# Performance work log

Measured on AMD Instinct MI355X. Metric: run time of the kernel, lower is better.

The kernel has to match this reference:

```python
import jax, jax.numpy as jnp
import numpy as np

E, C_IN, NUM_CLASSES = 4, 3, 100
HW = 32
C1, C2, GC = 64, 128, 16
FC_IN = C2 * (HW // 4) * (HW // 4)  # 128*8*8 = 8192


def _conv(x, w, b):
    # x: [B,Cin,H,W], w: [Cout,Cin,3,3] -> [B,Cout,H,W] (SAME padding)
    y = jax.lax.conv_general_dilated(x, w, (1, 1), 'SAME',
                                     dimension_numbers=('NCHW', 'OIHW', 'NCHW'))
    return y + b[None, :, None, None]


def _maxpool2(x):
    return jax.lax.reduce_window(x, -jnp.inf, jax.lax.max,
                                 (1, 1, 2, 2), (1, 1, 2, 2), 'VALID')


def setup_inputs() -> dict:
    key = jax.random.key(0)
    ks = jax.random.split(key, 12)
    s = lambda k, shape, fan: (jax.random.normal(k, shape, jnp.float32) / np.sqrt(fan))
    return {
        'x': jax.random.normal(ks[0], (1024, C_IN, HW, HW), jnp.float32),
        # gating network
        'gate_cw': s(ks[1], (GC, C_IN, 3, 3), C_IN * 9),
        'gate_cb': jnp.zeros((GC,), jnp.float32),
        'gate_fw': s(ks[2], (E, GC), GC),
        'gate_fb': jnp.zeros((E,), jnp.float32),
        # stacked expert params [E, ...]
        'e_c1w': s(ks[3], (E, C1, C_IN, 3, 3), C_IN * 9),
        'e_c1b': jnp.zeros((E, C1), jnp.float32),
        'e_c2w': s(ks[4], (E, C2, C1, 3, 3), C1 * 9),
        'e_c2b': jnp.zeros((E, C2), jnp.float32),
        'e_fw': s(ks[5], (E, NUM_CLASSES, FC_IN), FC_IN),
        'e_fb': jnp.zeros((E, NUM_CLASSES), jnp.float32),
    }


def reference(x, gate_cw, gate_cb, gate_fw, gate_fb,
              e_c1w, e_c1b, e_c2w, e_c2b, e_fw, e_fb):
    B = x.shape[0]
    # --- gating: conv -> relu -> global avg pool -> linear -> softmax ---
    g = jax.nn.relu(_conv(x, gate_cw, gate_cb))            # [B,GC,H,W]
    g = g.mean(axis=(2, 3))                                # [B,GC]
    router_probs = jax.nn.softmax(g @ gate_fw.T + gate_fb) # [B,E]

    best_weights = router_probs.max(axis=1)                # [B]
    best_indices = jnp.argmax(router_probs, axis=1)        # [B]

    # --- hard top-1 dispatch: mask-and-combine (same math as gather/scatter) ---
    final_output = jnp.zeros((B, NUM_CLASSES), x.dtype)
    for e in range(E):  # fixed small expert count, structurally distinct params
        h = jax.nn.relu(_conv(x, e_c1w[e], e_c1b[e]))      # [B,64,32,32]
        h = _maxpool2(h)                                   # [B,64,16,16]
        h = jax.nn.relu(_conv(h, e_c2w[e], e_c2b[e]))      # [B,128,16,16]
        h = _maxpool2(h)                                   # [B,128,8,8]
        logits = h.reshape(B, -1) @ e_fw[e].T + e_fb[e]    # [B,100]
        mask = (best_indices == e)[:, None]
        final_output = final_output + jnp.where(
            mask, logits * best_weights[:, None], 0.0)

    mean_probs = router_probs.mean(axis=0)
    aux_loss = jnp.mean((mean_probs - 1.0 / E) ** 2)
    return final_output, router_probs, aux_loss
```

## Files before the change

### kernel.cpp

```cpp
#include <hip/hip_runtime.h>
#include <hip/hip_bf16.h>
#include <cstdint>


#define B_TOT 1024

typedef __attribute__((ext_vector_type(8))) short short8;
typedef __attribute__((ext_vector_type(16))) float f32x16;

__device__ __forceinline__ ushort f2bf(float f) {
  uint32_t u = __float_as_uint(f);
  u += 0x7fffu + ((u >> 16) & 1u);
  return (ushort)(u >> 16);
}

__global__ __launch_bounds__(256) void k_prep(
    const float* __restrict__ x, const float* __restrict__ gcw,
    const float* __restrict__ gcb, float* __restrict__ g_mean,
    const float* __restrict__ w2, ushort* __restrict__ wp,
    const float* __restrict__ w1, ushort* __restrict__ wA,
    const float* __restrict__ efw, ushort* __restrict__ wfc) {
  __shared__ float xs[3 * 34 * 34];
  __shared__ float red[4 * 16];
  const int blk = blockIdx.x;
  const int t = threadIdx.x;

  if (blk < 1024) {
    const int b = blk;
    const float* xb = x + (size_t)b * 3072;

    for (int c = t; c < 3468; c += 256) {
      const int ci = c / 1156;
      const int rem = c - ci * 1156;
      const int y = rem / 34;
      const int xx = rem - y * 34;
      const int gy = y - 1, gx = xx - 1;
      float v = 0.f;
      if (gy >= 0 && gy < 32 && gx >= 0 && gx < 32) v = xb[ci * 1024 + gy * 32 + gx];
      xs[c] = v;
    }
    __syncthreads();

    const int r = t >> 3;
    const int c0 = (t & 7) * 4;

    float accp[16][4];
#pragma unroll
    for (int c = 0; c < 16; c++)
#pragma unroll
      for (int p = 0; p < 4; p++) accp[c][p] = 0.f;

#pragma unroll
    for (int ci = 0; ci < 3; ci++) {
      float pv[3][6];
#pragma unroll
      for (int dy = 0; dy < 3; dy++) {
        const float* row = xs + ci * 1156 + (r + dy) * 34 + c0;
#pragma unroll
        for (int dx = 0; dx < 6; dx++) pv[dy][dx] = row[dx];
      }
#pragma unroll
      for (int c = 0; c < 16; c++) {
        const float* wr = gcw + (c * 3 + ci) * 9;
#pragma unroll
        for (int ky = 0; ky < 3; ky++)
#pragma unroll
          for (int kx = 0; kx < 3; kx++) {
            const float wv = wr[ky * 3 + kx];
#pragma unroll
            for (int p = 0; p < 4; p++)
              accp[c][p] += wv * pv[ky][kx + p];
          }
      }
    }

    float sums[16];
#pragma unroll
    for (int c = 0; c < 16; c++) {
      const float bb = gcb[c];
      float s = 0.f;
#pragma unroll
      for (int p = 0; p < 4; p++) s += fmaxf(accp[c][p] + bb, 0.f);
      sums[c] = s;
    }

    const int wave = t >> 6, lane = t & 63;
#pragma unroll
    for (int c = 0; c < 16; c++) {
      float v = sums[c];
      for (int o = 32; o > 0; o >>= 1) v += __shfl_down(v, o);
      if (lane == 0) red[wave * 16 + c] = v;
    }
    __syncthreads();
    if (t < 16) {
      g_mean[b * 16 + t] =
          (red[t] + red[16 + t] + red[32 + t] + red[48 + t]) * (1.f / 1024.f);
    }
  } else if (blk < 2176) {
    const int i = (blk - 1024) * 256 + t;
    const int j = i & 7;
    const int cout = (i >> 3) & 127;
    const int kb = (i >> 10) & 7;
    const int kkE = i >> 13;
    const int kk = kkE - (kkE / 9) * 9;
    const int e = kkE / 9;
    const int ci = kb * 8 + j;
    const float f = w2[(size_t)(((e * 128 + cout) * 64 + ci) * 9) + kk];
    wp[i] = f2bf(f);
  } else if (blk < 2304) {
    const int i = (blk - 2176) * 256 + t;
    const int j = i & 7;
    const int cout = (i >> 3) & 63;
    const int kb = (i >> 9) & 3;
    const int e = i >> 11;
    const int k = kb * 8 + j;
    float f = 0.f;
    if (k < 27) {
      const int ci = k / 9;
      const int kk = k - ci * 9;
      f = w1[(size_t)(((e * 64 + cout) * 3 + ci) * 9) + kk];
    }
    wA[i] = f2bf(f);
  } else {
    const int i = (blk - 2304) * 256 + t;
    const int j = i & 7;
    const int cout = (i >> 3) & 127;
    const int kb = (i >> 10) & 1023;
    const int e = i >> 20;
    const int k = kb * 8 + j;
    float f = 0.f;
    if (cout < 100) f = efw[((size_t)(e * 100 + cout)) * 8192 + k];
    wfc[i] = f2bf(f);
  }
}

__global__ __launch_bounds__(256) void k_route(
    const float* __restrict__ g_mean, const float* __restrict__ gfw,
    const float* __restrict__ gfb, float* __restrict__ probs,
    float* __restrict__ best_w, int* __restrict__ best_idx,
    int* __restrict__ off_g, int* __restrict__ counts_g,
    int* __restrict__ order, float* __restrict__ aux_out) {
  __shared__ int cnt[4], ofs[5], cl[4];
  __shared__ short bidx[1024];
  __shared__ float red[16];
  const int t = threadIdx.x;
  if (t < 4) { cnt[t] = 0; cl[t] = 0; }
  __syncthreads();

  float asum[4] = {0.f, 0.f, 0.f, 0.f};
  for (int s = t; s < B_TOT; s += 256) {
    float g[16];
#pragma unroll
    for (int c = 0; c < 16; c++) g[c] = g_mean[s * 16 + c];
    float lg[4];
#pragma unroll
    for (int e = 0; e < 4; e++) {
      float sum = gfb[e];
#pragma unroll
      for (int c = 0; c < 16; c++) sum += g[c] * gfw[e * 16 + c];
      lg[e] = sum;
    }
    const float m = fmaxf(fmaxf(lg[0], lg[1]), fmaxf(lg[2], lg[3]));
    float ex[4], ssum = 0.f;
#pragma unroll
    for (int e = 0; e < 4; e++) { ex[e] = expf(lg[e] - m); ssum += ex[e]; }
    const float inv = 1.f / ssum;
    float p[4];
#pragma unroll
    for (int e = 0; e < 4; e++) {
      p[e] = ex[e] * inv;
      probs[s * 4 + e] = p[e];
      asum[e] += p[e];
    }
    int bi = 0; float bp = p[0];
#pragma unroll
    for (int e = 1; e < 4; e++) if (p[e] > bp) { bp = p[e]; bi = e; }
    best_w[s] = bp;
    best_idx[s] = bi;
    bidx[s] = (short)bi;
    atomicAdd(&cnt[bi], 1);
  }
  __syncthreads();

  if (t == 0) {
    int o = 0;
#pragma unroll
    for (int e = 0; e < 4; e++) { ofs[e] = o; o += ((cnt[e] + 31) & ~31); }
    ofs[4] = o;
#pragma unroll
    for (int i = 0; i < 5; i++) off_g[i] = ofs[i];
#pragma unroll
    for (int e = 0; e < 4; e++) counts_g[e] = cnt[e];
  }
  __syncthreads();

  for (int s = t; s < B_TOT; s += 256) {
    const int e2 = bidx[s];
    const int slot = ofs[e2] + atomicAdd(&cl[e2], 1);
    order[slot] = s;
  }

  const int wave = t >> 6, lane = t & 63;
#pragma unroll
  for (int e = 0; e < 4; e++) {
    float v = asum[e];
    for (int o = 32; o > 0; o >>= 1) v += __shfl_down(v, o);
    if (lane == 0) red[wave * 4 + e] = v;
  }
  __syncthreads();
  if (t == 0) {
    float aux = 0.f;
#pragma unroll
    for (int e = 0; e < 4; e++) {
      const float mp = (red[e] + red[4 + e] + red[8 + e] + red[12 + e]) * (1.f / 1024.f);
      const float d = mp - 0.25f;
      aux += d * d;
    }
    aux_out[0] = aux * 0.25f;
  }
}

__global__ __launch_bounds__(256) void k_conv1(
    const float* __restrict__ x, const ushort* __restrict__ wA,
    const float* __restrict__ b1, const int* __restrict__ best_idx,
    ushort* __restrict__ h1q) {
  __shared__ ushort xs[1020];
  __shared__ __align__(16) ushort Bl[256 * 32];
  const int blk = blockIdx.x;
  const int b = blk >> 2;
  const int q = blk & 3;
  const int t = threadIdx.x;
  const int e = __builtin_amdgcn_readfirstlane(best_idx[b]);
  const float* xb = x + (size_t)b * 3072;
  const float* b1e = b1 + (size_t)e * 64;

  for (int c = t; c < 1020; c += 256) {
    const int ci = c / 340;
    const int rem = c - ci * 340;
    const int hr = rem / 34;
    const int hc = rem - hr * 34;
    const int gr = 8 * q + hr - 1, gc = hc - 1;
    float v = 0.f;
    if (gr >= 0 && gr < 32 && gc >= 0 && gc < 32) v = xb[ci * 1024 + gr * 32 + gc];
    xs[c] = f2bf(v);
  }
  __syncthreads();

  {
    const int rr = t >> 5, cc = t & 31;
    ushort us[32];
#pragma unroll
    for (int k = 0; k < 32; k++) {
      ushort v = 0;
      if (k < 27) {
        const int ci = k / 9;
        const int tap = k - ci * 9;
        const int dy = tap / 3, dx = tap - dy * 3;
        v = xs[ci * 340 + (rr + dy) * 34 + cc + dx];
      }
      us[k] = v;
    }
    uint4 pk[2];
    uint* pu = (uint*)pk;
#pragma unroll
    for (int w = 0; w < 8; w++)
      pu[w] = (uint)us[w * 2] | ((uint)us[w * 2 + 1] << 16);
    *(uint4*)(Bl + t * 32) = pk[0];
    *(uint4*)(Bl + t * 32 + 8) = pk[1];
    uint4 pk2[2];
    uint* pu2 = (uint*)pk2;
#pragma unroll
    for (int w = 0; w < 8; w++)
      pu2[w] = (uint)us[16 + w * 2] | ((uint)us[16 + w * 2 + 1] << 16);
    *(uint4*)(Bl + t * 32 + 16) = pk2[0];
    *(uint4*)(Bl + t * 32 + 24) = pk2[1];
  }
  __syncthreads();

  const int lane = t & 63;
  const int wv = t >> 6;
  const int g = wv & 1;
  const int nh = wv >> 1;
  const int ln = lane & 31;
  const int half = lane >> 5;

  const short8 af0 = *(const short8*)(wA + (size_t)(((e * 4 + half) * 64) + g * 32 + ln) * 8);
  const short8 af1 = *(const short8*)(wA + (size_t)(((e * 4 + 2 + half) * 64) + g * 32 + ln) * 8);

  f32x16 acc[4];
#pragma unroll
  for (int tt = 0; tt < 4; tt++)
#pragma unroll
    for (int i = 0; i < 16; i++) acc[tt][i] = 0.f;

#pragma unroll
  for (int tt = 0; tt < 4; tt++) {
    const ushort* bcol = Bl + (size_t)((nh * 4 + tt) * 32 + ln) * 32;
    const short8 b0 = *(const short8*)(bcol + half * 8);
    const short8 b1v = *(const short8*)(bcol + 16 + half * 8);
    acc[tt] = __builtin_amdgcn_mfma_f32_32x32x16_bf16(af0, b0, acc[tt], 0, 0, 0);
    acc[tt] = __builtin_amdgcn_mfma_f32_32x32x16_bf16(af1, b1v, acc[tt], 0, 0, 0);
  }

  float bias[16];
#pragma unroll
  for (int r = 0; r < 16; r++)
    bias[r] = b1e[g * 32 + (r & 3) + 8 * (r >> 2) + 4 * half];

  const int pc = ln >> 1;
#pragma unroll
  for (int j = 0; j < 2; j++) {
    float pw[16];
#pragma unroll
    for (int r = 0; r < 16; r++) {
      float v = fmaxf(acc[2 * j][r], acc[2 * j + 1][r]);
      v = fmaxf(v, __shfl_xor(v, 1));
      pw[r] = fmaxf(v + bias[r], 0.f);
    }
    if ((lane & 1) == 0) {
      const int pos = (4 * q + nh * 2 + j) * 16 + pc;
      ushort* dst = h1q + (size_t)b * 16384 + pos * 8 + 4 * half;
#pragma unroll
      for (int rg = 0; rg < 4; rg++) {
        uint2 pk;
        pk.x = (uint)f2bf(pw[rg * 4 + 0]) | ((uint)f2bf(pw[rg * 4 + 1]) << 16);
        pk.y = (uint)f2bf(pw[rg * 4 + 2]) | ((uint)f2bf(pw[rg * 4 + 3]) << 16);
        *(uint2*)(dst + (g * 4 + rg) * 2048) = pk;
      }
    }
  }
}

__global__ __launch_bounds__(512, 2) void k_conv2(
    const ushort* __restrict__ h1q, const ushort* __restrict__ wp,
    const float* __restrict__ b2, const int* __restrict__ best_idx,
    ushort* __restrict__ h2q) {
  __shared__ uint4 st[1440];
  const int blk = blockIdx.x;
  const int b = blk >> 1;
  const int q = blk & 1;
  const int t = threadIdx.x;
  const int e = __builtin_amdgcn_readfirstlane(best_idx[b]);
  const ushort* wpe = wp + (size_t)e * 73728;

  for (int c = t; c < 1440; c += 512) {
    const int row = c / 144;
    const int rem = c - row * 144;
    const int cig = rem / 18;
    const int col = rem - cig * 18;
    const int gy = 8 * q - 1 + row, gx = col - 1;
    uint4 v = make_uint4(0u, 0u, 0u, 0u);
    if (gy >= 0 && gy < 16 && gx >= 0 && gx < 16)
      v = *(const uint4*)(h1q + (size_t)b * 16384 + cig * 2048 + (gy * 16 + gx) * 8);
    st[c] = v;
  }
  __syncthreads();

  const int lane = t & 63;
  const int wv = t >> 6;
  const int g = wv & 1;
  const int h = wv >> 1;
  const int half = lane >> 5;
  const int n = lane & 31;
  const int drow = n >> 4;
  const int col15 = n & 15;
  const int cm0 = g * 64;

  const short* sbs = (const short*)st;
  const ushort* abase = wpe + (size_t)(half * 128 + cm0 + n) * 8;

  f32x16 acc[2];
#pragma unroll
  for (int m = 0; m < 2; m++)
#pragma unroll
    for (int i = 0; i < 16; i++) acc[m][i] = 0.f;

  short8 a0[4], a1[4];
#pragma unroll
  for (int c4 = 0; c4 < 4; c4++) {
    a0[c4] = *(const short8*)(abase + c4 * 2048);
    a1[c4] = *(const short8*)(abase + c4 * 2048 + 256);
  }

#pragma unroll
  for (int kk = 0; kk < 9; kk++) {
    const int ky = kk / 3;
    const int kx = kk - ky * 3;
#pragma unroll
    for (int c4 = 0; c4 < 4; c4++) {
      const int kb = c4 * 2 + half;
      const int rin = 2 * h + drow + ky;
      const int cin = col15 + kx;
      const short8 bf = *(const short8*)(sbs + ((rin * 8 + kb) * 18 + cin) * 8);
      acc[0] = __builtin_amdgcn_mfma_f32_32x32x16_bf16(a0[c4], bf, acc[0], 0, 0, 0);
      acc[1] = __builtin_amdgcn_mfma_f32_32x32x16_bf16(a1[c4], bf, acc[1], 0, 0, 0);
      if (kk < 8) {
        a0[c4] = *(const short8*)(abase + (kk + 1) * 8192 + c4 * 2048);
        a1[c4] = *(const short8*)(abase + (kk + 1) * 8192 + c4 * 2048 + 256);
      }
    }
  }
  __syncthreads();

  ushort* pls = (ushort*)st;
#pragma unroll
  for (int m = 0; m < 2; m++) {
#pragma unroll
    for (int r = 0; r < 16; r++) {
      float v = acc[m][r];
      v = fmaxf(v, __shfl_xor(v, 1));
      v = fmaxf(v, __shfl_xor(v, 16));
      if ((lane & 17) == 0) {
        const int rowm = (r & 3) + 8 * (r >> 2) + 4 * half;
        const int cout = cm0 + m * 32 + rowm;
        const int prl = h;
        const int pc = (n >> 1) & 7;
        pls[cout * 32 + prl * 8 + pc] = f2bf(fmaxf(v + b2[e * 128 + cout], 0.f));
      }
    }
  }
  __syncthreads();

  {
    const int f16 = t;
    const int flat = f16 * 8;
    const int cout = flat >> 5;
    const int pos32 = flat & 31;
    uint4* dst = (uint4*)(h2q + (size_t)b * 8192 + cout * 64 + 32 * q + pos32);
    *dst = ((const uint4*)pls)[f16];
  }
}

__global__ __launch_bounds__(256) void k_fc(
    const ushort* __restrict__ h2q, const ushort* __restrict__ wfc,
    const int* __restrict__ order, const int* __restrict__ off,
    const int* __restrict__ counts, float* __restrict__ partial) {
  __shared__ ushort bs[32 * 32 * 8];
  __shared__ int sid[32];
  const int tix = blockIdx.x;
  const int ks = blockIdx.y;
  const int base = tix * 32;
  if (base >= off[4]) return;
  int e = 0;
#pragma unroll
  for (int i = 1; i < 4; i++) if (base >= off[i]) e = i;
  const int vend = off[e] + counts[e];
  const int t = threadIdx.x;
  if (t < 32) {
    const int pos = base + t;
    sid[t] = (pos < vend) ? order[pos] : -1;
  }
  __syncthreads();

  const int lane = t & 63;
  const int wv = t >> 6;
  const int half = lane >> 5;
  const int mn = lane & 31;
  const int cout0 = wv * 32;
  const int ss = t & 31;
  const int kgrp = t >> 5;
  const int srow = sid[ss] >= 0 ? sid[ss] : 0;
  const ushort* arow = h2q + (size_t)srow * 8192;

  f32x16 acc;
#pragma unroll
  for (int i = 0; i < 16; i++) acc[i] = 0.f;

  const ushort* wbase = wfc + ((size_t)e * 1024 + (size_t)ks * 64) * 1024;
  const short* sb = (const short*)bs;

#pragma unroll
  for (int ch = 0; ch < 2; ch++) {
    const int k0g = ks * 512 + ch * 256;
    if (ch) __syncthreads();
#pragma unroll
    for (int p = 0; p < 4; p++) {
      const int kb = p * 8 + kgrp;
      const uint4 v = *(const uint4*)(arow + k0g + kb * 8);
      *(uint4*)(bs + (kb * 32 + ss) * 8) = v;
    }
    __syncthreads();
#pragma unroll
    for (int kk = 0; kk < 16; kk++) {
      const int kbl = kk * 2 + half;
      const short8 af = *(const short8*)(wbase +
          ((size_t)(ch * 32 + kbl) * 128 + cout0 + mn) * 8);
      const short8 bf = *(const short8*)(sb + (kbl * 32 + mn) * 8);
      acc = __builtin_amdgcn_mfma_f32_32x32x16_bf16(af, bf, acc, 0, 0, 0);
    }
  }

  float* pks = partial + (size_t)ks * 147456;
#pragma unroll
  for (int r = 0; r < 16; r++) {
    const int cout = cout0 + (r & 3) + 8 * (r >> 2) + 4 * half;
    pks[(size_t)cout * 1152 + base + mn] = acc[r];
  }
}

__global__ __launch_bounds__(256) void k_red(
    const float* __restrict__ partial, const float* __restrict__ efb,
    const int* __restrict__ order, const int* __restrict__ off,
    const int* __restrict__ counts, const float* __restrict__ best_w,
    float* __restrict__ out) {
  const int slot = blockIdx.x * 256 + threadIdx.x;
  if (slot >= off[4]) return;
  int e = 0;
#pragma unroll
  for (int i = 1; i < 4; i++) if (slot >= off[i]) e = i;
  if (slot - off[e] >= counts[e]) return;
  const int s = order[slot];
  const float bw = best_w[s];
  const int o0 = blockIdx.y * 4;
#pragma unroll
  for (int j = 0; j < 4; j++) {
    const int o = o0 + j;
    float sum = 0.f;
#pragma unroll
    for (int ks = 0; ks < 16; ks++)
      sum += partial[(size_t)ks * 147456 + (size_t)o * 1152 + slot];
    out[(size_t)s * 100 + o] = (sum + efb[e * 100 + o]) * bw;
  }
}

extern "C" void kernel_launch(void* const* d_in, const int* in_sizes, int n_in,
                              void* d_out, int out_size, void* d_ws, size_t ws_size,
                              hipStream_t stream) {
  const float* x   = (const float*)d_in[0];
  const float* gcw = (const float*)d_in[1];
  const float* gcb = (const float*)d_in[2];
  const float* gfw = (const float*)d_in[3];
  const float* gfb = (const float*)d_in[4];
  const float* c1w = (const float*)d_in[5];
  const float* c1b = (const float*)d_in[6];
  const float* c2w = (const float*)d_in[7];
  const float* c2b = (const float*)d_in[8];
  const float* efw = (const float*)d_in[9];
  const float* efb = (const float*)d_in[10];
  float* out = (float*)d_out;
  float* ws  = (float*)d_ws;

  float*  g_mean   = ws;
  float*  best_w   = ws + 16384;
  int*    best_idx = (int*)(ws + 17408);
  int*    counts   = (int*)(ws + 18432);
  int*    off      = (int*)(ws + 18440);
  int*    order    = (int*)(ws + 18448);
  ushort* wp       = (ushort*)(ws + 20480);
  ushort* wfc      = (ushort*)(ws + 167936);
  ushort* h1       = (ushort*)(ws + 2265088);
  ushort* h2q      = (ushort*)(ws + 10653696);
  float*  partial  = ws + 14848000;
  ushort* wA       = (ushort*)(ws + 17207296);

  float* probs = out + 102400;
  float* aux   = out + 106496;

  k_prep<<<18688, 256, 0, stream>>>(x, gcw, gcb, g_mean, c2w, wp, c1w, wA, efw, wfc);
  k_route<<<1, 256, 0, stream>>>(g_mean, gfw, gfb, probs, best_w, best_idx,
                                 off, counts, order, aux);
  k_conv1<<<4096, 256, 0, stream>>>(x, wA, c1b, best_idx, h1);
  k_conv2<<<2048, 512, 0, stream>>>(h1, wp, c2b, best_idx, h2q);
  dim3 g5(36, 16);
  k_fc<<<g5, 256, 0, stream>>>(h2q, wfc, order, off, counts, partial);
  dim3 g6(5, 25);
  k_red<<<g6, 256, 0, stream>>>(partial, efb, order, off, counts, best_w, out);
}
```

Measured before the change: 215.9 us.

## Fuse gating softmax into prep kernel and merge conv1 row-quarter blocks per sample

The per-sample router linear layer, softmax and argmax move into the prep kernel's gating blocks, so the single-block route kernel only counts experts, builds the order and computes aux loss instead of doing the dense routing math serially. conv1 now launches one block per sample that stages the full padded image in LDS once and loops over four row strips, rather than four blocks that each reload overlapping halo rows. This cuts serial work in a one-block kernel and redundant global loads, but conv1 has a quarter as many blocks, which lowers parallelism and adds barriers inside the loop.

```diff
diff --git a/kernel.cpp b/kernel.cpp
--- a/kernel.cpp
+++ b/kernel.cpp
@@ -16,12 +16,16 @@
 
 __global__ __launch_bounds__(256) void k_prep(
     const float* __restrict__ x, const float* __restrict__ gcw,
-    const float* __restrict__ gcb, float* __restrict__ g_mean,
+    const float* __restrict__ gcb, const float* __restrict__ gfw,
+    const float* __restrict__ gfb, float* __restrict__ probs,
+    float* __restrict__ best_w, int* __restrict__ best_idx,
     const float* __restrict__ w2, ushort* __restrict__ wp,
     const float* __restrict__ w1, ushort* __restrict__ wA,
     const float* __restrict__ efw, ushort* __restrict__ wfc) {
   __shared__ float xs[3 * 34 * 34];
   __shared__ float red[4 * 16];
+  __shared__ float gm[16];
+  __shared__ float lgs[4];
   const int blk = blockIdx.x;
   const int t = threadIdx.x;
 
@@ -92,9 +96,29 @@
       if (lane == 0) red[wave * 16 + c] = v;
     }
     __syncthreads();
-    if (t < 16) {
-      g_mean[b * 16 + t] =
-          (red[t] + red[16 + t] + red[32 + t] + red[48 + t]) * (1.f / 1024.f);
+    if (t < 16)
+      gm[t] = (red[t] + red[16 + t] + red[32 + t] + red[48 + t]) * (1.f / 1024.f);
+    __syncthreads();
+    if (t < 4) {
+      float sum = gfb[t];
+#pragma unroll
+      for (int c = 0; c < 16; c++) sum += gm[c] * gfw[t * 16 + c];
+      lgs[t] = sum;
+    }
+    __syncthreads();
+    if (t == 0) {
+      const float m = fmaxf(fmaxf(lgs[0], lgs[1]), fmaxf(lgs[2], lgs[3]));
+      float ex[4], ssum = 0.f;
+#pragma unroll
+      for (int e = 0; e < 4; e++) { ex[e] = __expf(lgs[e] - m); ssum += ex[e]; }
+      const float inv = 1.f / ssum;
+      int bi = 0; float bp = ex[0];
+#pragma unroll
+      for (int e = 1; e < 4; e++) if (ex[e] > bp) { bp = ex[e]; bi = e; }
+#pragma unroll
+      for (int e = 0; e < 4; e++) probs[b * 4 + e] = ex[e] * inv;
+      best_w[b] = bp * inv;
+      best_idx[b] = bi;
     }
   } else if (blk < 2176) {
     const int i = (blk - 1024) * 256 + t;
@@ -135,9 +159,7 @@
 }
 
 __global__ __launch_bounds__(256) void k_route(
-    const float* __restrict__ g_mean, const float* __restrict__ gfw,
-    const float* __restrict__ gfb, float* __restrict__ probs,
-    float* __restrict__ best_w, int* __restrict__ best_idx,
+    const float* __restrict__ probs, const int* __restrict__ best_idx_g,
     int* __restrict__ off_g, int* __restrict__ counts_g,
     int* __restrict__ order, float* __restrict__ aux_out) {
   __shared__ int cnt[4], ofs[5], cl[4];
@@ -149,36 +171,11 @@
 
   float asum[4] = {0.f, 0.f, 0.f, 0.f};
   for (int s = t; s < B_TOT; s += 256) {
-    float g[16];
-#pragma unroll
-    for (int c = 0; c < 16; c++) g[c] = g_mean[s * 16 + c];
-    float lg[4];
-#pragma unroll
-    for (int e = 0; e < 4; e++) {
-      float sum = gfb[e];
-#pragma unroll
-      for (int c = 0; c < 16; c++) sum += g[c] * gfw[e * 16 + c];
-      lg[e] = sum;
-    }
-    const float m = fmaxf(fmaxf(lg[0], lg[1]), fmaxf(lg[2], lg[3]));
-    float ex[4], ssum = 0.f;
-#pragma unroll
-    for (int e = 0; e < 4; e++) { ex[e] = expf(lg[e] - m); ssum += ex[e]; }
-    const float inv = 1.f / ssum;
-    float p[4];
-#pragma unroll
-    for (int e = 0; e < 4; e++) {
-      p[e] = ex[e] * inv;
-      probs[s * 4 + e] = p[e];
-      asum[e] += p[e];
-    }
-    int bi = 0; float bp = p[0];
-#pragma unroll
-    for (int e = 1; e < 4; e++) if (p[e] > bp) { bp = p[e]; bi = e; }
-    best_w[s] = bp;
-    best_idx[s] = bi;
+    const int bi = best_idx_g[s];
     bidx[s] = (short)bi;
     atomicAdd(&cnt[bi], 1);
+#pragma unroll
+    for (int e = 0; e < 4; e++) asum[e] += probs[s * 4 + e];
   }
   __syncthreads();
 
@@ -224,58 +221,24 @@
     const float* __restrict__ x, const ushort* __restrict__ wA,
     const float* __restrict__ b1, const int* __restrict__ best_idx,
     ushort* __restrict__ h1q) {
-  __shared__ ushort xs[1020];
+  __shared__ ushort xs[3 * 34 * 34];
   __shared__ __align__(16) ushort Bl[256 * 32];
-  const int blk = blockIdx.x;
-  const int b = blk >> 2;
-  const int q = blk & 3;
+  const int b = blockIdx.x;
   const int t = threadIdx.x;
   const int e = __builtin_amdgcn_readfirstlane(best_idx[b]);
   const float* xb = x + (size_t)b * 3072;
   const float* b1e = b1 + (size_t)e * 64;
 
-  for (int c = t; c < 1020; c += 256) {
-    const int ci = c / 340;
-    const int rem = c - ci * 340;
-    const int hr = rem / 34;
-    const int hc = rem - hr * 34;
-    const int gr = 8 * q + hr - 1, gc = hc - 1;
+  for (int c = t; c < 3468; c += 256) {
+    const int ci = c / 1156;
+    const int rem = c - ci * 1156;
+    const int y = rem / 34;
+    const int xx = rem - y * 34;
+    const int gy = y - 1, gx = xx - 1;
     float v = 0.f;
-    if (gr >= 0 && gr < 32 && gc >= 0 && gc < 32) v = xb[ci * 1024 + gr * 32 + gc];
+    if (gy >= 0 && gy < 32 && gx >= 0 && gx < 32) v = xb[ci * 1024 + gy * 32 + gx];
     xs[c] = f2bf(v);
   }
-  __syncthreads();
-
-  {
-    const int rr = t >> 5, cc = t & 31;
-    ushort us[32];
-#pragma unroll
-    for (int k = 0; k < 32; k++) {
-      ushort v = 0;
-      if (k < 27) {
-        const int ci = k / 9;
-        const int tap = k - ci * 9;
-        const int dy = tap / 3, dx = tap - dy * 3;
-        v = xs[ci * 340 + (rr + dy) * 34 + cc + dx];
-      }
-      us[k] = v;
-    }
-    uint4 pk[2];
-    uint* pu = (uint*)pk;
-#pragma unroll
-    for (int w = 0; w < 8; w++)
-      pu[w] = (uint)us[w * 2] | ((uint)us[w * 2 + 1] << 16);
-    *(uint4*)(Bl + t * 32) = pk[0];
-    *(uint4*)(Bl + t * 32 + 8) = pk[1];
-    uint4 pk2[2];
-    uint* pu2 = (uint*)pk2;
-#pragma unroll
-    for (int w = 0; w < 8; w++)
-      pu2[w] = (uint)us[16 + w * 2] | ((uint)us[16 + w * 2 + 1] << 16);
-    *(uint4*)(Bl + t * 32 + 16) = pk2[0];
-    *(uint4*)(Bl + t * 32 + 24) = pk2[1];
-  }
-  __syncthreads();
 
   const int lane = t & 63;
   const int wv = t >> 6;
@@ -283,49 +246,84 @@
   const int nh = wv >> 1;
   const int ln = lane & 31;
   const int half = lane >> 5;
+  const int rr = t >> 5, cc = t & 31;
 
   const short8 af0 = *(const short8*)(wA + (size_t)(((e * 4 + half) * 64) + g * 32 + ln) * 8);
   const short8 af1 = *(const short8*)(wA + (size_t)(((e * 4 + 2 + half) * 64) + g * 32 + ln) * 8);
 
-  f32x16 acc[4];
-#pragma unroll
-  for (int tt = 0; tt < 4; tt++)
-#pragma unroll
-    for (int i = 0; i < 16; i++) acc[tt][i] = 0.f;
-
-#pragma unroll
-  for (int tt = 0; tt < 4; tt++) {
-    const ushort* bcol = Bl + (size_t)((nh * 4 + tt) * 32 + ln) * 32;
-    const short8 b0 = *(const short8*)(bcol + half * 8);
-    const short8 b1v = *(const short8*)(bcol + 16 + half * 8);
-    acc[tt] = __builtin_amdgcn_mfma_f32_32x32x16_bf16(af0, b0, acc[tt], 0, 0, 0);
-    acc[tt] = __builtin_amdgcn_mfma_f32_32x32x16_bf16(af1, b1v, acc[tt], 0, 0, 0);
-  }
-
   float bias[16];
 #pragma unroll
   for (int r = 0; r < 16; r++)
     bias[r] = b1e[g * 32 + (r & 3) + 8 * (r >> 2) + 4 * half];
 
-  const int pc = ln >> 1;
-#pragma unroll
-  for (int j = 0; j < 2; j++) {
-    float pw[16];
-#pragma unroll
-    for (int r = 0; r < 16; r++) {
-      float v = fmaxf(acc[2 * j][r], acc[2 * j + 1][r]);
-      v = fmaxf(v, __shfl_xor(v, 1));
-      pw[r] = fmaxf(v + bias[r], 0.f);
-    }
-    if ((lane & 1) == 0) {
-      const int pos = (4 * q + nh * 2 + j) * 16 + pc;
-      ushort* dst = h1q + (size_t)b * 16384 + pos * 8 + 4 * half;
-#pragma unroll
-      for (int rg = 0; rg < 4; rg++) {
-        uint2 pk;
-        pk.x = (uint)f2bf(pw[rg * 4 + 0]) | ((uint)f2bf(pw[rg * 4 + 1]) << 16);
-        pk.y = (uint)f2bf(pw[rg * 4 + 2]) | ((uint)f2bf(pw[rg * 4 + 3]) << 16);
-        *(uint2*)(dst + (g * 4 + rg) * 2048) = pk;
+#pragma unroll 1
+  for (int s = 0; s < 4; s++) {
+    __syncthreads();
+    {
+      ushort us[32];
+#pragma unroll
+      for (int k = 0; k < 32; k++) {
+        ushort v = 0;
+        if (k < 27) {
+          const int ci = k / 9;
+          const int tap = k - ci * 9;
+          const int dy = tap / 3, dx = tap - dy * 3;
+          v = xs[ci * 1156 + (8 * s + rr + dy) * 34 + cc + dx];
+        }
+        us[k] = v;
+      }
+      uint4 pk[2];
+      uint* pu = (uint*)pk;
+#pragma unroll
+      for (int w = 0; w < 8; w++)
+        pu[w] = (uint)us[w * 2] | ((uint)us[w * 2 + 1] << 16);
+      *(uint4*)(Bl + t * 32) = pk[0];
+      *(uint4*)(Bl + t * 32 + 8) = pk[1];
+      uint4 pk2[2];
+      uint* pu2 = (uint*)pk2;
+#pragma unroll
+      for (int w = 0; w < 8; w++)
+        pu2[w] = (uint)us[16 + w * 2] | ((uint)us[16 + w * 2 + 1] << 16);
+      *(uint4*)(Bl + t * 32 + 16) = pk2[0];
+      *(uint4*)(Bl + t * 32 + 24) = pk2[1];
+    }
+    __syncthreads();
+
+    f32x16 acc[4];
+#pragma unroll
+    for (int tt = 0; tt < 4; tt++)
+#pragma unroll
+      for (int i = 0; i < 16; i++) acc[tt][i] = 0.f;
+
+#pragma unroll
+    for (int tt = 0; tt < 4; tt++) {
+      const ushort* bcol = Bl + (size_t)((nh * 4 + tt) * 32 + ln) * 32;
+      const short8 b0 = *(const short8*)(bcol + half * 8);
+      const short8 b1v = *(const short8*)(bcol + 16 + half * 8);
+      acc[tt] = __builtin_amdgcn_mfma_f32_32x32x16_bf16(af0, b0, acc[tt], 0, 0, 0);
+      acc[tt] = __builtin_amdgcn_mfma_f32_32x32x16_bf16(af1, b1v, acc[tt], 0, 0, 0);
+    }
+
+    const int pc = ln >> 1;
+#pragma unroll
+    for (int j = 0; j < 2; j++) {
+      float pw[16];
+#pragma unroll
+      for (int r = 0; r < 16; r++) {
+        float v = fmaxf(acc[2 * j][r], acc[2 * j + 1][r]);
+        v = fmaxf(v, __shfl_xor(v, 1));
+        pw[r] = fmaxf(v + bias[r], 0.f);
+      }
+      if ((lane & 1) == 0) {
+        const int pos = (4 * s + nh * 2 + j) * 16 + pc;
+        ushort* dst = h1q + (size_t)b * 16384 + pos * 8 + 4 * half;
+#pragma unroll
+        for (int rg = 0; rg < 4; rg++) {
+          uint2 pk;
+          pk.x = (uint)f2bf(pw[rg * 4 + 0]) | ((uint)f2bf(pw[rg * 4 + 1]) << 16);
+          pk.y = (uint)f2bf(pw[rg * 4 + 2]) | ((uint)f2bf(pw[rg * 4 + 3]) << 16);
+          *(uint2*)(dst + (g * 4 + rg) * 2048) = pk;
+        }
       }
     }
   }
@@ -540,7 +538,6 @@
   float* out = (float*)d_out;
   float* ws  = (float*)d_ws;
 
-  float*  g_mean   = ws;
   float*  best_w   = ws + 16384;
   int*    best_idx = (int*)(ws + 17408);
   int*    counts   = (int*)(ws + 18432);
@@ -556,10 +553,10 @@
   float* probs = out + 102400;
   float* aux   = out + 106496;
 
-  k_prep<<<18688, 256, 0, stream>>>(x, gcw, gcb, g_mean, c2w, wp, c1w, wA, efw, wfc);
-  k_route<<<1, 256, 0, stream>>>(g_mean, gfw, gfb, probs, best_w, best_idx,
-                                 off, counts, order, aux);
-  k_conv1<<<4096, 256, 0, stream>>>(x, wA, c1b, best_idx, h1);
+  k_prep<<<18688, 256, 0, stream>>>(x, gcw, gcb, gfw, gfb, probs, best_w,
+                                    best_idx, c2w, wp, c1w, wA, efw, wfc);
+  k_route<<<1, 256, 0, stream>>>(probs, best_idx, off, counts, order, aux);
+  k_conv1<<<1024, 256, 0, stream>>>(x, wA, c1b, best_idx, h1);
   k_conv2<<<2048, 512, 0, stream>>>(h1, wp, c2b, best_idx, h2q);
   dim3 g5(36, 16);
   k_fc<<<g5, 256, 0, stream>>>(h2q, wfc, order, off, counts, partial);
```

New measurement: 216.7 us. About the same (+0.4%).
